# Kernel optimization log

Measured on AMD Instinct MI355X. Metric: run time of the kernel, lower is better.

## Reference

```python
import jax, jax.numpy as jnp
import numpy as np

B, S, D = 2, 4096, 768
H, W = 12, 128          # W = one-sided attention window; S % (2*W) == 0
DFF = 3072
HD = D // H
EPS = 1e-6


def band_attention(q, k, v, w):
    """Sliding-window (banded) attention, sliding_chunks-equivalent.
    q,k,v: (B, S, H, HD); q pre-scaled by 1/sqrt(HD).
    Returns context (B, S, D) and band probs (B, H, S, 2w+1)."""
    b, s, h, hd = q.shape
    n = s // w                                    # number of query blocks
    qb = q.reshape(b, n, w, h, hd)
    kp = jnp.pad(k, ((0, 0), (w, w), (0, 0), (0, 0)))   # zero-pad seq by w each side
    vp = jnp.pad(v, ((0, 0), (w, w), (0, 0), (0, 0)))
    # block i needs padded keys [i*w, i*w + 3w)  (blocks i-1, i, i+1)
    gidx = jnp.arange(n)[:, None] * w + jnp.arange(3 * w)[None, :]   # (n, 3w)
    kb = kp[:, gidx]                              # (b, n, 3w, h, hd)
    vb = vp[:, gidx]
    scores = jnp.einsum('bnthd,bnjhd->bhntj', qb, kb)   # (b,h,n,w,3w)
    t = jnp.arange(w)[:, None]                    # (w,1) pos within block
    j = jnp.arange(3 * w)[None, :]                # (1,3w)
    rel = j - w - t                               # relative key offset, valid in [-w,w]
    pos = jnp.arange(n)[:, None, None] * w + (j - w)     # (n,1,3w) global key pos
    valid = (jnp.abs(rel) <= w)[None] & (pos >= 0) & (pos < s)  # (n,w,3w)
    scores = jnp.where(valid[None, None], scores, -jnp.inf)
    probs = jax.nn.softmax(scores, axis=-1)
    out = jnp.einsum('bhntj,bnjhd->bnthd', probs, vb).reshape(b, s, h * hd)
    # extract the (2w+1) diagonals: offset d -> column j = t + d
    jj = jnp.arange(w)[:, None] + jnp.arange(2 * w + 1)[None, :]     # (w, 2w+1)
    attw = jnp.take_along_axis(probs, jj[None, None, None], axis=-1)
    return out, attw.reshape(b, h, s, 2 * w + 1)


def setup_inputs() -> dict:
    key = jax.random.key(0)
    ks = jax.random.split(key, 12)
    def lin(k, fan_in, shape):
        return (jax.random.normal(k, shape, jnp.float32) / np.sqrt(fan_in)).astype(jnp.float32)
    return {
        'src': jax.random.normal(ks[0], (B, S, D), jnp.float32),
        'Wq': lin(ks[1], D, (D, D)), 'bq': jnp.zeros((D,), jnp.float32),
        'Wk': lin(ks[2], D, (D, D)), 'bk': jnp.zeros((D,), jnp.float32),
        'Wv': lin(ks[3], D, (D, D)), 'bv': jnp.zeros((D,), jnp.float32),
        'W1': lin(ks[4], D, (D, DFF)), 'b1': jnp.zeros((DFF,), jnp.float32),
        'W2': lin(ks[5], DFF, (DFF, D)), 'b2': jnp.zeros((D,), jnp.float32),
        'g2': 1.0 + 0.1 * jax.random.normal(ks[6], (D,), jnp.float32),
        'beta2': 0.1 * jax.random.normal(ks[7], (D,), jnp.float32),
    }


def reference(src, Wq, bq, Wk, bk, Wv, bv, W1, b1, W2, b2, g2, beta2):
    b, s, d = src.shape
    # self-attention (allenai LongformerSelfAttention: q/k/v linears, no out proj)
    q = ((src @ Wq + bq) / np.sqrt(HD).astype(np.float32)).reshape(b, s, H, HD)
    k = (src @ Wk + bk).reshape(b, s, H, HD)
    v = (src @ Wv + bv).reshape(b, s, H, HD)
    attn_out, attn_w = band_attention(q, k, v, W)
    x = src + attn_out                      # residual (dropout=0, eval)
    # PositionalwiseFeedForward: Linear -> ReLU -> Linear
    ffn = jnp.maximum(x @ W1 + b1, 0.0) @ W2 + b2
    y = x + ffn
    # post-norm (normalize_before=False: only norm2 is applied)
    mu = jnp.mean(y, axis=-1, keepdims=True)
    var = jnp.mean(jnp.square(y - mu), axis=-1, keepdims=True)
    out = g2 * (y - mu) / jnp.sqrt(var + EPS) + beta2
    return out, attn_w
```

## Files before the change

kernel.cpp:

```cpp
#include <hip/hip_runtime.h>
#include <hip/hip_bf16.h>
#include <stdint.h>

#define NB 2
#define NS 4096
#define ND 768
#define NH 12
#define NW 128
#define NDFF 3072
#define NHD 64
#define NCH 32

typedef __attribute__((ext_vector_type(8))) short bf16x8;
typedef __attribute__((ext_vector_type(4))) short s16x4;
typedef __attribute__((ext_vector_type(4))) float f32x4;

__device__ __forceinline__ float bf2f(short u) {
    union { unsigned int i; float f; } c;
    c.i = ((unsigned int)(unsigned short)u) << 16;
    return c.f;
}
__device__ __forceinline__ short f2bf(float f) {
    union { float f; unsigned int i; } c;
    c.f = f;
    unsigned int x = c.i;
    return (short)((x + 0x7fffu + ((x >> 16) & 1u)) >> 16);
}

__device__ __forceinline__ void gl16(const void* g, const void* l) {
    __builtin_amdgcn_global_load_lds(
        (const __attribute__((address_space(1))) void*)g,
        (__attribute__((address_space(3))) void*)l, 16, 0, 0);
}

__global__ __launch_bounds__(256) void cast_bf16(const float* __restrict__ in,
                                                 short* __restrict__ out, int n4) {
    int i = blockIdx.x * 256 + threadIdx.x;
    if (i < n4) {
        f32x4 v = ((const f32x4*)in)[i];
        s16x4 o;
        o[0] = f2bf(v[0]); o[1] = f2bf(v[1]); o[2] = f2bf(v[2]); o[3] = f2bf(v[3]);
        ((s16x4*)out)[i] = o;
    }
}

__global__ __launch_bounds__(256) void transpose_cast(const float* __restrict__ in,
                                                      short* __restrict__ out,
                                                      int K, int N) {
    __shared__ float tile[32][33];
    int kb = blockIdx.y * 32, nb = blockIdx.x * 32;
    int tx = threadIdx.x & 31, ty = threadIdx.x >> 5;
    #pragma unroll
    for (int r = ty; r < 32; r += 8)
        tile[r][tx] = in[(long)(kb + r) * N + nb + tx];
    __syncthreads();
    #pragma unroll
    for (int r = ty; r < 32; r += 8)
        out[(long)(nb + r) * K + kb + tx] = f2bf(tile[tx][r]);
}

template<int MODE>
__global__ __launch_bounds__(256, 2) void gemmdb(
    const short* __restrict__ A,
    const short* __restrict__ Bt,
    const float* __restrict__ b0,
    const float* __restrict__ b1,
    const float* __restrict__ b2,
    void* __restrict__ outp,
    const float* __restrict__ xres,
    int M, int N, int K, int gx)
{
    __shared__ short lds[2][256 * 64];
    const int KT = K >> 6;

    int cpx = gridDim.x >> 3;
    int bid = blockIdx.x;
    int tile = (bid & 7) * cpx + (bid >> 3);
    int n0 = (tile % gx) * 128;
    int m0 = (tile / gx) * 128;

    int tid = threadIdx.x;
    int wid = tid >> 6, lane = tid & 63;
    int wr = wid >> 1, wc = wid & 1;
    int g = lane >> 4, lr = lane & 15;

    int rl = lane >> 3, sl = lane & 7;
    int soff = (sl ^ rl) << 3;
    const short* gA[4];
    const short* gB[4];
    #pragma unroll
    for (int c = 0; c < 4; ++c) {
        int row = c * 32 + wid * 8 + rl;
        gA[c] = A + (long)(m0 + row) * K + soff;
        gB[c] = Bt + (long)(n0 + row) * K + soff;
    }

    f32x4 acc[4][4];
    #pragma unroll
    for (int a = 0; a < 4; ++a)
        #pragma unroll
        for (int c = 0; c < 4; ++c)
            acc[a][c] = (f32x4){0.f, 0.f, 0.f, 0.f};

    auto stage = [&](int t, int buf) {
        long ko = (long)t << 6;
        #pragma unroll
        for (int c = 0; c < 4; ++c) {
            int lbase = (c * 32 + wid * 8) * 64;
            gl16(gA[c] + ko, &lds[buf][lbase]);
            gl16(gB[c] + ko, &lds[buf][128 * 64 + lbase]);
        }
    };

    stage(0, 0);
    asm volatile("s_waitcnt vmcnt(0)" ::: "memory");
    __builtin_amdgcn_s_barrier();

    int buf = 0;
    for (int t = 0; t < KT; ++t) {
        if (t + 1 < KT) stage(t + 1, buf ^ 1);
        const short* bufA = lds[buf];
        const short* bufB = lds[buf] + 128 * 64;
        bf16x8 af[2][4], bfr[2][4];
        #pragma unroll
        for (int kk = 0; kk < 2; ++kk) {
            int ph = (((kk << 2) + g) ^ (lr & 7)) << 3;
            #pragma unroll
            for (int mt = 0; mt < 4; ++mt)
                af[kk][mt] = *(const bf16x8*)&bufA[(wr * 64 + mt * 16 + lr) * 64 + ph];
            #pragma unroll
            for (int nt = 0; nt < 4; ++nt)
                bfr[kk][nt] = *(const bf16x8*)&bufB[(wc * 64 + nt * 16 + lr) * 64 + ph];
        }
        #pragma unroll
        for (int kk = 0; kk < 2; ++kk)
            #pragma unroll
            for (int mt = 0; mt < 4; ++mt)
                #pragma unroll
                for (int nt = 0; nt < 4; ++nt)
                    acc[mt][nt] = __builtin_amdgcn_mfma_f32_16x16x32_bf16(
                        af[kk][mt], bfr[kk][nt], acc[mt][nt], 0, 0, 0);
        asm volatile("s_waitcnt vmcnt(0)" ::: "memory");
        __builtin_amdgcn_s_barrier();
        buf ^= 1;
    }

    int mr0 = m0 + wr * 64;
    int nc0 = n0 + wc * 64;
    if (MODE == 4) {
        int proj = n0 / 768;
        const float* bp = (proj == 0) ? b0 : (proj == 1) ? b1 : b2;
        float scl = (proj == 0) ? 0.125f : 1.0f;
        short* obase = (short*)outp + (long)proj * ((long)NB * NS * ND);
        #pragma unroll
        for (int mt = 0; mt < 4; ++mt) {
            #pragma unroll
            for (int nt = 0; nt < 4; ++nt) {
                int c = nc0 + nt * 16 + lr - proj * 768;
                int hh = c >> 6, hd = c & 63;
                float bv = bp[c];
                if (proj == 2) {
                    int m = mr0 + mt * 16 + (g << 2);
                    int bbi = m >> 12, s = m & (NS - 1);
                    s16x4 ov;
                    ov[0] = f2bf(acc[mt][nt][0] + bv);
                    ov[1] = f2bf(acc[mt][nt][1] + bv);
                    ov[2] = f2bf(acc[mt][nt][2] + bv);
                    ov[3] = f2bf(acc[mt][nt][3] + bv);
                    *(s16x4*)&obase[((long)(bbi * NH + hh) * NHD + hd) * NS + s] = ov;
                } else {
                    #pragma unroll
                    for (int i = 0; i < 4; ++i) {
                        int m = mr0 + mt * 16 + (g << 2) + i;
                        int bbi = m >> 12, s = m & (NS - 1);
                        obase[((long)(bbi * NH + hh) * NS + s) * NHD + hd] =
                            f2bf((acc[mt][nt][i] + bv) * scl);
                    }
                }
            }
        }
    } else {
        #pragma unroll
        for (int mt = 0; mt < 4; ++mt) {
            #pragma unroll
            for (int nt = 0; nt < 4; ++nt) {
                int col = nc0 + nt * 16 + lr;
                float bv = b0[col];
                #pragma unroll
                for (int i = 0; i < 4; ++i) {
                    int m = mr0 + mt * 16 + (g << 2) + i;
                    float v = acc[mt][nt][i];
                    if (MODE == 2) {
                        v = fmaxf(v + bv, 0.f);
                        ((short*)outp)[(long)m * NDFF + col] = f2bf(v);
                    } else {
                        v = v + bv + xres[(long)m * ND + col];
                        ((float*)outp)[(long)m * ND + col] = v;
                    }
                }
            }
        }
    }
}

#define KLD 72
#define PLD 392
#define ATT_LDS (384 * KLD * 2 + 128 * PLD * 2)

__global__ __launch_bounds__(512) void attn_kernel(
    const short* __restrict__ qg,
    const short* __restrict__ kg,
    const short* __restrict__ vtg,
    const float* __restrict__ src,
    float* __restrict__ attw,
    float* __restrict__ x,
    short* __restrict__ xb)
{
    extern __shared__ char smem[];
    short* kv = (short*)smem;
    short* pl = (short*)(smem + 384 * KLD * 2);

    int blk = blockIdx.x;
    int ch = blk & 31;
    int tmp = blk >> 5;
    int h = tmp % NH;
    int b = tmp / NH;
    int tid = threadIdx.x;
    int wid = tid >> 6;
    int lane = tid & 63;
    int g = lane >> 4, lr = lane & 15;
    long bh = (long)(b * NH + h);
    long kbase = bh * NS * NHD;
    int srow0 = ch * NW;

    #pragma unroll
    for (int it = 0; it < 6; ++it) {
        int idx = it * 512 + tid;
        int j = idx >> 3;
        int c = (idx & 7) << 3;
        int s = srow0 - NW + j;
        bf16x8 v = {};
        if (s >= 0 && s < NS)
            v = *(const bf16x8*)&kg[kbase + (long)s * NHD + c];
        *(bf16x8*)&kv[j * KLD + c] = v;
    }

    bf16x8 vreg[6];
    #pragma unroll
    for (int it = 0; it < 6; ++it) {
        int idx = it * 512 + tid;
        int hd = idx / 48;
        int c = (idx % 48) << 3;
        int s0 = srow0 - NW + c;
        bf16x8 v = {};
        if (s0 >= 0 && s0 < NS)
            v = *(const bf16x8*)&vtg[(bh * NHD + hd) * NS + s0];
        vreg[it] = v;
    }

    int t0 = wid << 4;
    bf16x8 aq[2];
    #pragma unroll
    for (int kk = 0; kk < 2; ++kk)
        aq[kk] = *(const bf16x8*)&qg[kbase + (long)(srow0 + t0 + lr) * NHD + (kk << 5) + (g << 3)];

    __syncthreads();

    f32x4 sc[24];
    #pragma unroll
    for (int jt = 0; jt < 24; ++jt) {
        f32x4 a = (f32x4){0.f, 0.f, 0.f, 0.f};
        #pragma unroll
        for (int kk = 0; kk < 2; ++kk) {
            bf16x8 bk = *(const bf16x8*)&kv[(jt * 16 + lr) * KLD + (kk << 5) + (g << 3)];
            a = __builtin_amdgcn_mfma_f32_16x16x32_bf16(aq[kk], bk, a, 0, 0, 0);
        }
        sc[jt] = a;
    }

    float mx[4] = {-3.0e30f, -3.0e30f, -3.0e30f, -3.0e30f};
    #pragma unroll
    for (int jt = 0; jt < 24; ++jt) {
        int j = jt * 16 + lr;
        int sp = srow0 - NW + j;
        bool pok = (sp >= 0) && (sp < NS);
        #pragma unroll
        for (int i = 0; i < 4; ++i) {
            int t = t0 + (g << 2) + i;
            bool ok = pok && (j >= t) && (j <= t + 2 * NW);
            float v = ok ? sc[jt][i] : -3.0e30f;
            sc[jt][i] = v;
            mx[i] = fmaxf(mx[i], v);
        }
    }
    #pragma unroll
    for (int m = 1; m < 16; m <<= 1) {
        #pragma unroll
        for (int i = 0; i < 4; ++i)
            mx[i] = fmaxf(mx[i], __shfl_xor(mx[i], m, 64));
    }
    float sm[4] = {0.f, 0.f, 0.f, 0.f};
    #pragma unroll
    for (int jt = 0; jt < 24; ++jt) {
        #pragma unroll
        for (int i = 0; i < 4; ++i) {
            float v = sc[jt][i];
            float p = (v > -1.0e30f) ? __expf(v - mx[i]) : 0.0f;
            sc[jt][i] = p;
            sm[i] += p;
        }
    }
    #pragma unroll
    for (int m = 1; m < 16; m <<= 1) {
        #pragma unroll
        for (int i = 0; i < 4; ++i)
            sm[i] += __shfl_xor(sm[i], m, 64);
    }
    float inv[4];
    #pragma unroll
    for (int i = 0; i < 4; ++i) inv[i] = 1.0f / sm[i];

    long aw = (bh * NS + srow0) * 257;
    #pragma unroll
    for (int jt = 0; jt < 24; ++jt) {
        int j = jt * 16 + lr;
        #pragma unroll
        for (int i = 0; i < 4; ++i) {
            int t = t0 + (g << 2) + i;
            float pv = sc[jt][i] * inv[i];
            pl[t * PLD + j] = f2bf(pv);
            int c = j - t;
            if (c >= 0 && c <= 2 * NW)
                attw[aw + (long)t * 257 + c] = pv;
        }
    }

    asm volatile("s_waitcnt lgkmcnt(0)" ::: "memory");
    __builtin_amdgcn_s_barrier();
    __builtin_amdgcn_sched_barrier(0);

    #pragma unroll
    for (int it = 0; it < 6; ++it) {
        int idx = it * 512 + tid;
        int hd = idx / 48;
        int c = (idx % 48) << 3;
        *(bf16x8*)&kv[hd * PLD + c] = vreg[it];
    }

    asm volatile("s_waitcnt lgkmcnt(0)" ::: "memory");
    __builtin_amdgcn_s_barrier();
    __builtin_amdgcn_sched_barrier(0);

    f32x4 o[4];
    #pragma unroll
    for (int nt = 0; nt < 4; ++nt) o[nt] = (f32x4){0.f, 0.f, 0.f, 0.f};
    #pragma unroll
    for (int kt = 0; kt < 12; ++kt) {
        bf16x8 ap = *(const bf16x8*)&pl[(t0 + lr) * PLD + (kt << 5) + (g << 3)];
        #pragma unroll
        for (int nt = 0; nt < 4; ++nt) {
            bf16x8 bv = *(const bf16x8*)&kv[(nt * 16 + lr) * PLD + (kt << 5) + (g << 3)];
            o[nt] = __builtin_amdgcn_mfma_f32_16x16x32_bf16(ap, bv, o[nt], 0, 0, 0);
        }
    }

    #pragma unroll
    for (int nt = 0; nt < 4; ++nt) {
        int d = nt * 16 + lr;
        int dcol = h * NHD + d;
        #pragma unroll
        for (int i = 0; i < 4; ++i) {
            int t = t0 + (g << 2) + i;
            long row = (long)b * NS + srow0 + t;
            float v = o[nt][i] + src[row * ND + dcol];
            x[row * ND + dcol] = v;
            xb[row * ND + dcol] = f2bf(v);
        }
    }
}

__global__ __launch_bounds__(256) void ln_kernel(float* __restrict__ y,
                                                 const float* __restrict__ g2,
                                                 const float* __restrict__ beta2) {
    int row = blockIdx.x;
    long base = (long)row * ND;
    int tid = threadIdx.x;
    float v[3];
    float s = 0.f, ss = 0.f;
    #pragma unroll
    for (int i = 0; i < 3; ++i) {
        v[i] = y[base + i * 256 + tid];
        s += v[i];
        ss += v[i] * v[i];
    }
    #pragma unroll
    for (int m = 1; m < 64; m <<= 1) {
        s += __shfl_xor(s, m, 64);
        ss += __shfl_xor(ss, m, 64);
    }
    __shared__ float red[8];
    int wid = tid >> 6, lane = tid & 63;
    if (lane == 0) { red[wid] = s; red[wid + 4] = ss; }
    __syncthreads();
    s = red[0] + red[1] + red[2] + red[3];
    ss = red[4] + red[5] + red[6] + red[7];
    float mu = s * (1.0f / ND);
    float var = ss * (1.0f / ND) - mu * mu;
    float rstd = rsqrtf(var + 1e-6f);
    #pragma unroll
    for (int i = 0; i < 3; ++i) {
        int c = i * 256 + tid;
        y[base + c] = g2[c] * (v[i] - mu) * rstd + beta2[c];
    }
}

extern "C" void kernel_launch(void* const* d_in, const int* in_sizes, int n_in,
                              void* d_out, int out_size, void* d_ws, size_t ws_size,
                              hipStream_t stream) {
    const float* src  = (const float*)d_in[0];
    const float* Wq   = (const float*)d_in[1];
    const float* bq   = (const float*)d_in[2];
    const float* Wk   = (const float*)d_in[3];
    const float* bk   = (const float*)d_in[4];
    const float* Wv   = (const float*)d_in[5];
    const float* bv   = (const float*)d_in[6];
    const float* W1   = (const float*)d_in[7];
    const float* b1   = (const float*)d_in[8];
    const float* W2   = (const float*)d_in[9];
    const float* b2   = (const float*)d_in[10];
    const float* g2   = (const float*)d_in[11];
    const float* bt2  = (const float*)d_in[12];

    float* out  = (float*)d_out;
    float* attw = out + (long)NB * NS * ND;

    char* ws = (char*)d_ws;
    const size_t SZ_XF  = (size_t)NB * NS * ND * 4;
    const size_t SZ_XB  = (size_t)NB * NS * ND * 2;
    const size_t SZ_W1T = (size_t)ND * NDFF * 2;
    const size_t SZ_W2T = (size_t)NDFF * ND * 2;
    const size_t SZ_QKV = (size_t)NB * NS * ND * 2;
    const size_t SZ_WT  = (size_t)ND * ND * 2;

    float* x_f32 = (float*)ws;
    short* x_bf  = (short*)(ws + SZ_XF);
    short* W1T   = (short*)(ws + SZ_XF + SZ_XB);
    short* W2T   = (short*)(ws + SZ_XF + SZ_XB + SZ_W1T);
    char*  regA  = ws + SZ_XF + SZ_XB + SZ_W1T + SZ_W2T;
    short* srcb  = (short*)regA;
    short* WqT   = (short*)(regA + SZ_QKV);
    short* WkT   = (short*)(regA + SZ_QKV + SZ_WT);
    short* WvT   = (short*)(regA + SZ_QKV + 2 * SZ_WT);
    short* qb    = (short*)(regA + SZ_QKV + 3 * SZ_WT);
    short* kb_   = (short*)(regA + 2 * SZ_QKV + 3 * SZ_WT);
    short* vb_   = (short*)(regA + 3 * SZ_QKV + 3 * SZ_WT);
    short* hbuf  = (short*)regA;

    const int M = NB * NS;

    cast_bf16<<<(M * ND / 4 + 255) / 256, 256, 0, stream>>>(src, srcb, M * ND / 4);
    transpose_cast<<<dim3(ND / 32, ND / 32), 256, 0, stream>>>(Wq, WqT, ND, ND);
    transpose_cast<<<dim3(ND / 32, ND / 32), 256, 0, stream>>>(Wk, WkT, ND, ND);
    transpose_cast<<<dim3(ND / 32, ND / 32), 256, 0, stream>>>(Wv, WvT, ND, ND);
    transpose_cast<<<dim3(NDFF / 32, ND / 32), 256, 0, stream>>>(W1, W1T, ND, NDFF);
    transpose_cast<<<dim3(ND / 32, NDFF / 32), 256, 0, stream>>>(W2, W2T, NDFF, ND);

    gemmdb<4><<<(2304 / 128) * (M / 128), 256, 0, stream>>>(
        srcb, WqT, bq, bk, bv, qb, nullptr, M, 2304, ND, 2304 / 128);

    (void)hipFuncSetAttribute(reinterpret_cast<const void*>(attn_kernel),
                              hipFuncAttributeMaxDynamicSharedMemorySize, ATT_LDS);
    attn_kernel<<<NB * NH * NCH, 512, ATT_LDS, stream>>>(qb, kb_, vb_, src, attw, x_f32, x_bf);

    gemmdb<2><<<(NDFF / 128) * (M / 128), 256, 0, stream>>>(
        x_bf, W1T, b1, b1, b1, hbuf, nullptr, M, NDFF, ND, NDFF / 128);
    gemmdb<3><<<(ND / 128) * (M / 128), 256, 0, stream>>>(
        hbuf, W2T, b2, b2, b2, out, x_f32, M, ND, NDFF, ND / 128);

    ln_kernel<<<M, 256, 0, stream>>>(out, g2, bt2);
}
```

Measured before the change: 254.2 us.

## Keep attention probs in registers, vectorize attw stores, drop fp32 residual buffer

The attention kernel now computes transposed scores (K as the A operand), so each lane owns one query row. This lets the softmax reductions use two shuffles instead of sixteen and lets band probabilities be written to attw as 16-byte vector stores. The bf16 probabilities are repacked through lane shuffles into the PV MFMA operand, so the P staging area in LDS is gone and more blocks can fit per CU. The fp32 residual buffer x is also dropped, and the W2 GEMM epilogue reads the bf16 copy instead. That saves a large global write and read but adds bf16 rounding to the residual path.

```diff
diff --git a/kernel.cpp b/kernel.cpp
--- a/kernel.cpp
+++ b/kernel.cpp
@@ -14,6 +14,7 @@
 typedef __attribute__((ext_vector_type(8))) short bf16x8;
 typedef __attribute__((ext_vector_type(4))) short s16x4;
 typedef __attribute__((ext_vector_type(4))) float f32x4;
+typedef __attribute__((ext_vector_type(4))) int i32x4;
 
 __device__ __forceinline__ float bf2f(short u) {
     union { unsigned int i; float f; } c;
@@ -25,6 +26,11 @@
     c.f = f;
     unsigned int x = c.i;
     return (short)((x + 0x7fffu + ((x >> 16) & 1u)) >> 16);
+}
+__device__ __forceinline__ unsigned int cvtpk(float lo, float hi) {
+    unsigned int r;
+    asm("v_cvt_pk_bf16_f32 %0, %1, %2" : "=v"(r) : "v"(lo), "v"(hi));
+    return r;
 }
 
 __device__ __forceinline__ void gl16(const void* g, const void* l) {
@@ -67,7 +73,7 @@
     const float* __restrict__ b1,
     const float* __restrict__ b2,
     void* __restrict__ outp,
-    const float* __restrict__ xres,
+    const short* __restrict__ xres,
     int M, int N, int K, int gx)
 {
     __shared__ short lds[2][256 * 64];
@@ -194,7 +200,7 @@
                         v = fmaxf(v + bv, 0.f);
                         ((short*)outp)[(long)m * NDFF + col] = f2bf(v);
                     } else {
-                        v = v + bv + xres[(long)m * ND + col];
+                        v = v + bv + bf2f(xres[(long)m * ND + col]);
                         ((float*)outp)[(long)m * ND + col] = v;
                     }
                 }
@@ -205,20 +211,18 @@
 
 #define KLD 72
 #define PLD 392
-#define ATT_LDS (384 * KLD * 2 + 128 * PLD * 2)
-
-__global__ __launch_bounds__(512) void attn_kernel(
+#define ATT_LDS (384 * KLD * 2)
+
+__global__ __launch_bounds__(512, 8) void attn_kernel(
     const short* __restrict__ qg,
     const short* __restrict__ kg,
     const short* __restrict__ vtg,
     const float* __restrict__ src,
     float* __restrict__ attw,
-    float* __restrict__ x,
     short* __restrict__ xb)
 {
     extern __shared__ char smem[];
     short* kv = (short*)smem;
-    short* pl = (short*)(smem + 384 * KLD * 2);
 
     int blk = blockIdx.x;
     int ch = blk & 31;
@@ -259,12 +263,15 @@
     }
 
     int t0 = wid << 4;
+    int tl = t0 + lr;
     bf16x8 aq[2];
     #pragma unroll
     for (int kk = 0; kk < 2; ++kk)
-        aq[kk] = *(const bf16x8*)&qg[kbase + (long)(srow0 + t0 + lr) * NHD + (kk << 5) + (g << 3)];
-
-    __syncthreads();
+        aq[kk] = *(const bf16x8*)&qg[kbase + (long)(srow0 + tl) * NHD + (kk << 5) + (g << 3)];
+
+    asm volatile("s_waitcnt lgkmcnt(0)" ::: "memory");
+    __builtin_amdgcn_s_barrier();
+    __builtin_amdgcn_sched_barrier(0);
 
     f32x4 sc[24];
     #pragma unroll
@@ -273,66 +280,63 @@
         #pragma unroll
         for (int kk = 0; kk < 2; ++kk) {
             bf16x8 bk = *(const bf16x8*)&kv[(jt * 16 + lr) * KLD + (kk << 5) + (g << 3)];
-            a = __builtin_amdgcn_mfma_f32_16x16x32_bf16(aq[kk], bk, a, 0, 0, 0);
+            a = __builtin_amdgcn_mfma_f32_16x16x32_bf16(bk, aq[kk], a, 0, 0, 0);
         }
         sc[jt] = a;
     }
 
-    float mx[4] = {-3.0e30f, -3.0e30f, -3.0e30f, -3.0e30f};
+    float mx = -3.0e30f;
     #pragma unroll
     for (int jt = 0; jt < 24; ++jt) {
-        int j = jt * 16 + lr;
-        int sp = srow0 - NW + j;
-        bool pok = (sp >= 0) && (sp < NS);
+        int j0 = jt * 16 + (g << 2);
         #pragma unroll
         for (int i = 0; i < 4; ++i) {
-            int t = t0 + (g << 2) + i;
-            bool ok = pok && (j >= t) && (j <= t + 2 * NW);
+            int j = j0 + i;
+            int sp = srow0 - NW + j;
+            bool ok = (sp >= 0) && (sp < NS) && (j >= tl) && (j <= tl + 2 * NW);
             float v = ok ? sc[jt][i] : -3.0e30f;
             sc[jt][i] = v;
-            mx[i] = fmaxf(mx[i], v);
-        }
-    }
-    #pragma unroll
-    for (int m = 1; m < 16; m <<= 1) {
-        #pragma unroll
-        for (int i = 0; i < 4; ++i)
-            mx[i] = fmaxf(mx[i], __shfl_xor(mx[i], m, 64));
-    }
-    float sm[4] = {0.f, 0.f, 0.f, 0.f};
+            mx = fmaxf(mx, v);
+        }
+    }
+    mx = fmaxf(mx, __shfl_xor(mx, 16, 64));
+    mx = fmaxf(mx, __shfl_xor(mx, 32, 64));
+    float sm = 0.f;
     #pragma unroll
     for (int jt = 0; jt < 24; ++jt) {
         #pragma unroll
         for (int i = 0; i < 4; ++i) {
             float v = sc[jt][i];
-            float p = (v > -1.0e30f) ? __expf(v - mx[i]) : 0.0f;
+            float p = (v > -1.0e30f) ? __expf(v - mx) : 0.0f;
             sc[jt][i] = p;
-            sm[i] += p;
-        }
-    }
-    #pragma unroll
-    for (int m = 1; m < 16; m <<= 1) {
-        #pragma unroll
-        for (int i = 0; i < 4; ++i)
-            sm[i] += __shfl_xor(sm[i], m, 64);
-    }
-    float inv[4];
-    #pragma unroll
-    for (int i = 0; i < 4; ++i) inv[i] = 1.0f / sm[i];
-
-    long aw = (bh * NS + srow0) * 257;
+            sm += p;
+        }
+    }
+    sm += __shfl_xor(sm, 16, 64);
+    sm += __shfl_xor(sm, 32, 64);
+    float inv = 1.0f / sm;
+
+    unsigned int pku[24][2];
+    long awrow = (bh * NS + srow0 + tl) * 257;
     #pragma unroll
     for (int jt = 0; jt < 24; ++jt) {
-        int j = jt * 16 + lr;
-        #pragma unroll
-        for (int i = 0; i < 4; ++i) {
-            int t = t0 + (g << 2) + i;
-            float pv = sc[jt][i] * inv[i];
-            pl[t * PLD + j] = f2bf(pv);
-            int c = j - t;
-            if (c >= 0 && c <= 2 * NW)
-                attw[aw + (long)t * 257 + c] = pv;
-        }
+        float pn[4];
+        #pragma unroll
+        for (int i = 0; i < 4; ++i) pn[i] = sc[jt][i] * inv;
+        int c0 = jt * 16 + (g << 2) - tl;
+        if (c0 >= 0 && c0 <= 2 * NW - 3) {
+            f32x4 vv = {pn[0], pn[1], pn[2], pn[3]};
+            *(f32x4*)&attw[awrow + c0] = vv;
+        } else {
+            #pragma unroll
+            for (int i = 0; i < 4; ++i) {
+                int c = c0 + i;
+                if (c >= 0 && c <= 2 * NW)
+                    attw[awrow + c] = pn[i];
+            }
+        }
+        pku[jt][0] = cvtpk(pn[0], pn[1]);
+        pku[jt][1] = cvtpk(pn[2], pn[3]);
     }
 
     asm volatile("s_waitcnt lgkmcnt(0)" ::: "memory");
@@ -351,16 +355,32 @@
     __builtin_amdgcn_s_barrier();
     __builtin_amdgcn_sched_barrier(0);
 
+    int lA = ((g & 1) << 5) + lr;
+    int lB = lA + 16;
+    bool hi = (g & 2) != 0;
     f32x4 o[4];
     #pragma unroll
     for (int nt = 0; nt < 4; ++nt) o[nt] = (f32x4){0.f, 0.f, 0.f, 0.f};
     #pragma unroll
     for (int kt = 0; kt < 12; ++kt) {
-        bf16x8 ap = *(const bf16x8*)&pl[(t0 + lr) * PLD + (kt << 5) + (g << 3)];
+        int a0 = __shfl((int)pku[2 * kt][0], lA, 64);
+        int a1 = __shfl((int)pku[2 * kt][1], lA, 64);
+        int a2 = __shfl((int)pku[2 * kt][0], lB, 64);
+        int a3 = __shfl((int)pku[2 * kt][1], lB, 64);
+        int b0 = __shfl((int)pku[2 * kt + 1][0], lA, 64);
+        int b1 = __shfl((int)pku[2 * kt + 1][1], lA, 64);
+        int b2 = __shfl((int)pku[2 * kt + 1][0], lB, 64);
+        int b3 = __shfl((int)pku[2 * kt + 1][1], lB, 64);
+        i32x4 wi;
+        wi[0] = hi ? b0 : a0;
+        wi[1] = hi ? b1 : a1;
+        wi[2] = hi ? b2 : a2;
+        wi[3] = hi ? b3 : a3;
+        bf16x8 af = *(bf16x8*)&wi;
         #pragma unroll
         for (int nt = 0; nt < 4; ++nt) {
             bf16x8 bv = *(const bf16x8*)&kv[(nt * 16 + lr) * PLD + (kt << 5) + (g << 3)];
-            o[nt] = __builtin_amdgcn_mfma_f32_16x16x32_bf16(ap, bv, o[nt], 0, 0, 0);
+            o[nt] = __builtin_amdgcn_mfma_f32_16x16x32_bf16(af, bv, o[nt], 0, 0, 0);
         }
     }
 
@@ -373,7 +393,6 @@
             int t = t0 + (g << 2) + i;
             long row = (long)b * NS + srow0 + t;
             float v = o[nt][i] + src[row * ND + dcol];
-            x[row * ND + dcol] = v;
             xb[row * ND + dcol] = f2bf(v);
         }
     }
@@ -442,7 +461,6 @@
     const size_t SZ_QKV = (size_t)NB * NS * ND * 2;
     const size_t SZ_WT  = (size_t)ND * ND * 2;
 
-    float* x_f32 = (float*)ws;
     short* x_bf  = (short*)(ws + SZ_XF);
     short* W1T   = (short*)(ws + SZ_XF + SZ_XB);
     short* W2T   = (short*)(ws + SZ_XF + SZ_XB + SZ_W1T);
@@ -470,12 +488,12 @@
 
     (void)hipFuncSetAttribute(reinterpret_cast<const void*>(attn_kernel),
                               hipFuncAttributeMaxDynamicSharedMemorySize, ATT_LDS);
-    attn_kernel<<<NB * NH * NCH, 512, ATT_LDS, stream>>>(qb, kb_, vb_, src, attw, x_f32, x_bf);
+    attn_kernel<<<NB * NH * NCH, 512, ATT_LDS, stream>>>(qb, kb_, vb_, src, attw, x_bf);
 
     gemmdb<2><<<(NDFF / 128) * (M / 128), 256, 0, stream>>>(
         x_bf, W1T, b1, b1, b1, hbuf, nullptr, M, NDFF, ND, NDFF / 128);
     gemmdb<3><<<(ND / 128) * (M / 128), 256, 0, stream>>>(
-        hbuf, W2T, b2, b2, b2, out, x_f32, M, ND, NDFF, ND / 128);
+        hbuf, W2T, b2, b2, b2, out, x_bf, M, ND, NDFF, ND / 128);
 
     ln_kernel<<<M, 256, 0, stream>>>(out, g2, bt2);
 }
```

Result: slower. 423.1 us (+66.5%).
